# Performance work log

Measured on AMD Instinct MI355X. Metric: run time of the kernel, lower is better.

Reference implementation:

```python
import jax, jax.numpy as jnp
import numpy as np

N, n, m, k = 100000, 32, 16, 32
MU = 100.0  # bubble kernel scale (init arg mu)


def setup_inputs() -> dict:
    key = jax.random.key(0)
    ks = jax.random.split(key, 7)
    x = jax.random.normal(ks[0], (N,), dtype=jnp.float32)
    # torch.nn.Linear(N, n): weight [n, N], bias [n]
    encoder_w = jax.random.normal(ks[1], (n, N), dtype=jnp.float32) / np.float32(np.sqrt(N))
    encoder_b = jnp.zeros((n,), dtype=jnp.float32)
    # decoder parameter [n, N]
    decoder = jax.random.normal(ks[2], (n, N), dtype=jnp.float32) / np.float32(np.sqrt(n))
    # torch.nn.Linear(n, n*m): weight [n*m, n], bias [n*m]
    bw_w = jax.random.normal(ks[3], (n * m, n), dtype=jnp.float32) / np.float32(np.sqrt(n))
    bw_b = jnp.zeros((n * m,), dtype=jnp.float32)
    neighbour_distance = jax.random.uniform(ks[4], (N, k), dtype=jnp.float32)
    neighbour_id = jax.random.randint(ks[5], (N, k), 0, N)
    clustering_labels = jax.random.randint(ks[6], (N,), 0, m)
    return {
        "x": x,
        "encoder_w": encoder_w,
        "encoder_b": encoder_b,
        "decoder": decoder,
        "bw_w": bw_w,
        "bw_b": bw_b,
        "neighbour_distance": neighbour_distance,
        "neighbour_id": neighbour_id,
        "clustering_labels": clustering_labels,
    }


def reference(x, encoder_w, encoder_b, decoder, bw_w, bw_b,
              neighbour_distance, neighbour_id, clustering_labels):
    # encode: [N] -> [n]
    encoded = x @ encoder_w.T + encoder_b
    # per-basis, per-cluster bandwidths: sigmoid(Linear)/60 -> [n, m] -> expand to [n, N]
    bandwidths = jax.nn.sigmoid(encoded @ bw_w.T + bw_b) / 60.0
    w = bandwidths.reshape(n, m)[:, clustering_labels]  # [n, N]
    # bubble window: relu(1 - d^2 / (w*mu)^2) -> [n, N, k]
    window = jax.nn.relu(1.0 - neighbour_distance[None, :, :] ** 2
                         / (w[:, :, None] * MU) ** 2)
    # normalization over axis 1 (the N axis), faithful to the source's dim=1
    window = window / jnp.sum(window, axis=1, keepdims=True)
    # gather decoder rows at neighbours, weight, reduce over k: [n, N]
    convolved_basis = jnp.sum(decoder[:, neighbour_id] * window, axis=-1)
    # [n] @ [n, N] -> [N]
    return encoded @ convolved_basis
```

## Files before the change

kernel.cpp:

```cpp
#include <hip/hip_runtime.h>
#include <hip/hip_fp16.h>

#define N_PTS 100000
#define MU_F  100.0f

typedef unsigned int uint;
typedef _Float16 h2 __attribute__((ext_vector_type(2)));
typedef float f2 __attribute__((ext_vector_type(2)));

#define E_SCALE 16384.0f
#define E_SCALE_INV (1.0f / 16384.0f)

static __device__ inline h2 h2pack(float a, float b) {
    return __builtin_bit_cast(h2, __builtin_amdgcn_cvt_pkrtz(a, b));
}
static __device__ inline float fdot2f(h2 a, h2 b, float c) {
    return __builtin_amdgcn_fdot2(a, b, c, false);
}
static __device__ inline h2 h2fma(h2 a, h2 b, h2 c) {
#if __has_builtin(__builtin_elementwise_fma)
    return __builtin_elementwise_fma(a, b, c);
#else
    return a * b + c;
#endif
}
static __device__ inline h2 h2max(h2 a, h2 b) {
#if __has_builtin(__builtin_elementwise_max)
    return __builtin_elementwise_max(a, b);
#else
    h2 r;
    r.x = a.x > b.x ? a.x : b.x;
    r.y = a.y > b.y ? a.y : b.y;
    return r;
#endif
}

#define ENC_BLKS 256
#define TR_BLKS  1563
#define S_BLKS   1024
#define S_PCH    98
#define NPAIRS   (N_PTS / 2)
#define M_BLKS   2048
#define M_CH     ((NPAIRS + M_BLKS - 1) / M_BLKS)

__global__ __launch_bounds__(256) void k_prep(const float* __restrict__ x,
                                              const float* __restrict__ encW,
                                              const float* __restrict__ encB,
                                              float* __restrict__ enc) {
    int b = blockIdx.x;
    int row = b & 31;
    int chunk = b >> 5;
    const int CH = N_PTS / 8;
    int base = chunk * CH;
    const float4* W4 = reinterpret_cast<const float4*>(encW + (size_t)row * N_PTS + base);
    const float4* x4 = reinterpret_cast<const float4*>(x + base);
    const int nv = CH / 4;
    float acc = 0.f;
    for (int idx = threadIdx.x; idx < nv; idx += 256) {
        float4 w = W4[idx];
        float4 xv = x4[idx];
        acc += w.x * xv.x + w.y * xv.y + w.z * xv.z + w.w * xv.w;
    }
    #pragma unroll
    for (int off = 32; off > 0; off >>= 1) acc += __shfl_down(acc, off);
    __shared__ float sred[4];
    int wid = threadIdx.x >> 6;
    if ((threadIdx.x & 63) == 0) sred[wid] = acc;
    __syncthreads();
    if (threadIdx.x == 0) {
        float s = sred[0] + sred[1] + sred[2] + sred[3];
        if (chunk == 0) s += encB[row];
        atomicAdd(enc + row, s);
    }
}

__global__ __launch_bounds__(256) void k_tab(const float* __restrict__ enc_g,
                                             const float* __restrict__ bw_w,
                                             const float* __restrict__ bw_b,
                                             float* __restrict__ invFG,
                                             h2* __restrict__ invHLG) {
    __shared__ float encL[32];
    __shared__ float invF[512];
    if (threadIdx.x < 32) encL[threadIdx.x] = enc_g[threadIdx.x];
    __syncthreads();
    for (int r = threadIdx.x; r < 512; r += 256) {
        int i = r >> 4, c = r & 15;
        const float4* wr4 = reinterpret_cast<const float4*>(bw_w + (size_t)r * 32);
        float z = bw_b[r];
        #pragma unroll
        for (int p4 = 0; p4 < 8; ++p4) {
            float4 wv = wr4[p4];
            z = fmaf(encL[4 * p4 + 0], wv.x, z);
            z = fmaf(encL[4 * p4 + 1], wv.y, z);
            z = fmaf(encL[4 * p4 + 2], wv.z, z);
            z = fmaf(encL[4 * p4 + 3], wv.w, z);
        }
        float s = 1.f / (1.f + __expf(-z));
        float wmu = s * (MU_F / 60.0f);
        float iv = 1.f / (wmu * wmu);
        invF[c * 32 + i] = iv;
        invFG[c * 32 + i] = iv;
    }
    __syncthreads();
    {
        int t = threadIdx.x;
        int c = t >> 4, q = (t >> 2) & 3, tt = t & 3;
        int i0 = q * 8 + 2 * tt;
        invHLG[t] = h2pack(fminf(invF[c * 32 + i0], 6.0e4f),
                           fminf(invF[c * 32 + i0 + 1], 6.0e4f));
    }
}

__global__ __launch_bounds__(256, 4) void k_S(const float* __restrict__ invFG,
                                              const float* __restrict__ nd,
                                              const int* __restrict__ labels,
                                              float* __restrict__ S,
                                              float* __restrict__ S_part,
                                              const float* __restrict__ dec,
                                              __half* __restrict__ decT) {
    int b = blockIdx.x;
    if (b >= S_BLKS) {
        __shared__ float tile[32][65];
        int j0 = (b - S_BLKS) * 64;
        int col = threadIdx.x & 63;
        int r0 = threadIdx.x >> 6;
        #pragma unroll
        for (int it = 0; it < 8; ++it) {
            int row = it * 4 + r0;
            int j = j0 + col;
            float v = (j < N_PTS) ? dec[(size_t)row * N_PTS + j] : 0.f;
            tile[row][col] = v;
        }
        __syncthreads();
        #pragma unroll
        for (int it = 0; it < 4; ++it) {
            int idx = it * 256 + threadIdx.x;
            int j = idx >> 4;
            int p = idx & 15;
            int jj = j0 + j;
            if (jj < N_PTS) {
                __half2 h = __halves2half2(__float2half(tile[2 * p][j]),
                                           __float2half(tile[2 * p + 1][j]));
                *reinterpret_cast<__half2*>(decT + (size_t)jj * 32 + 2 * p) = h;
            }
        }
        return;
    }

    __shared__ float invF[512];
    if (threadIdx.x < 128)
        reinterpret_cast<float4*>(invF)[threadIdx.x] =
            reinterpret_cast<const float4*>(invFG)[threadIdx.x];
    __syncthreads();

    int kk = threadIdx.x & 31;
    int ig = threadIdx.x >> 5;
    int start = b * S_PCH;
    int jend = min(start + S_PCH, N_PTS);

    float a0 = 0.f, a1 = 0.f, a2 = 0.f, a3 = 0.f;

    auto ld4 = [&](int jbase, float* d, int* cc) {
        #pragma unroll
        for (int u = 0; u < 4; ++u) {
            int j = jbase + u;
            int jc = min(j, N_PTS - 1);
            float dv = nd[(size_t)jc * 32 + kk];
            cc[u] = labels[jc];
            d[u] = (j < jend) ? dv : 1.0e15f;
        }
    };
    float dA[4], dB[4]; int cA[4], cB[4];
    ld4(start, dA, cA);
    for (int jj = start; jj < jend; jj += 4) {
        ld4(jj + 4, dB, cB);
        #pragma unroll
        for (int u = 0; u < 4; ++u) {
            float4 iv = *reinterpret_cast<const float4*>(&invF[cA[u] * 32 + ig * 4]);
            float d2 = dA[u] * dA[u];
            a0 += fmaxf(fmaf(d2, -iv.x, 1.f), 0.f);
            a1 += fmaxf(fmaf(d2, -iv.y, 1.f), 0.f);
            a2 += fmaxf(fmaf(d2, -iv.z, 1.f), 0.f);
            a3 += fmaxf(fmaf(d2, -iv.w, 1.f), 0.f);
        }
        #pragma unroll
        for (int u = 0; u < 4; ++u) { dA[u] = dB[u]; cA[u] = cB[u]; }
    }

    int cell = (ig * 4) * 32 + kk;
    if (S_part) {
        float* dst = S_part + (size_t)b * 1024 + cell;
        dst[0] = a0; dst[32] = a1; dst[64] = a2; dst[96] = a3;
    } else {
        atomicAdd(&S[cell], a0);
        atomicAdd(&S[cell + 32], a1);
        atomicAdd(&S[cell + 64], a2);
        atomicAdd(&S[cell + 96], a3);
    }
}

__global__ __launch_bounds__(1024) void k_S_reduce(const float* __restrict__ S_part,
                                                   float* __restrict__ S) {
    int g = blockIdx.x;
    int t = threadIdx.x;
    float s = 0.f;
    #pragma unroll
    for (int u = 0; u < 16; ++u)
        s += S_part[(size_t)(g * 16 + u) * 1024 + t];
    atomicAdd(&S[t], s);
}

__global__ __launch_bounds__(256) void k_elf(const float* __restrict__ enc_g,
                                             const float* __restrict__ S_g,
                                             h2* __restrict__ EhG_A,
                                             h2* __restrict__ EhG_B) {
    __shared__ float encL[32];
    __shared__ float ELf[1024];
    if (threadIdx.x < 32) encL[threadIdx.x] = enc_g[threadIdx.x];
    __syncthreads();
    for (int t = threadIdx.x; t < 1024; t += 256)
        ELf[t] = encL[t >> 5] / S_g[t] * E_SCALE;
    __syncthreads();
    {
        int t = threadIdx.x;
        int lane = t >> 2, tt = t & 3;
        int R = lane >> 2, q = lane & 3;
        int i0 = q * 8 + 2 * tt;
        EhG_A[t] = h2pack(ELf[i0 * 32 + R],      ELf[(i0 + 1) * 32 + R]);
        EhG_B[t] = h2pack(ELf[i0 * 32 + R + 16], ELf[(i0 + 1) * 32 + R + 16]);
    }
}

__global__ __launch_bounds__(256, 4) void k_main(const h2* __restrict__ invHLG,
                                                 const h2* __restrict__ EhG_A,
                                                 const h2* __restrict__ EhG_B,
                                                 const float* __restrict__ nd,
                                                 const int* __restrict__ nid,
                                                 const int* __restrict__ labels,
                                                 const __half* __restrict__ decT,
                                                 float* __restrict__ out) {
    __shared__ h2 invHL[256];
    if (threadIdx.x < 64)
        reinterpret_cast<uint4*>(invHL)[threadIdx.x] =
            reinterpret_cast<const uint4*>(invHLG)[threadIdx.x];
    __syncthreads();

    int lane = threadIdx.x & 63;
    int R = lane >> 2;
    int q = lane & 3;

    h2 EhA[4], EhB[4];
    {
        uint4 a = reinterpret_cast<const uint4*>(EhG_A)[lane];
        uint4 bq = reinterpret_cast<const uint4*>(EhG_B)[lane];
        EhA[0] = __builtin_bit_cast(h2, a.x);  EhA[1] = __builtin_bit_cast(h2, a.y);
        EhA[2] = __builtin_bit_cast(h2, a.z);  EhA[3] = __builtin_bit_cast(h2, a.w);
        EhB[0] = __builtin_bit_cast(h2, bq.x); EhB[1] = __builtin_bit_cast(h2, bq.y);
        EhB[2] = __builtin_bit_cast(h2, bq.z); EhB[3] = __builtin_bit_cast(h2, bq.w);
    }
    const h2 zero2 = h2pack(0.f, 0.f);
    const h2 one2 = h2pack(1.f, 1.f);

    int w = threadIdx.x >> 6;
    int start = blockIdx.x * M_CH;
    int pend = min(start + M_CH, NPAIRS);
    int pa = start + w;
    const uint4* decQ = reinterpret_cast<const uint4*>(decT);
    if (pa >= pend) return;

    auto load_ldd = [&](int pc, int* id, float* dd, int& c0, int& c1) {
        pc = min(pc, NPAIRS - 1);
        int j0 = 2 * pc, j1 = j0 + 1;
        #pragma unroll
        for (int s = 0; s < 4; ++s) {
            size_t idx = (size_t)((s >> 1) ? j1 : j0) * 32 + (s & 1) * 16 + R;
            id[s] = __builtin_nontemporal_load(&nid[idx]);
            dd[s] = __builtin_nontemporal_load(&nd[idx]);
        }
        c0 = labels[j0];
        c1 = labels[j1];
    };
    auto load_rows = [&](const int* id, uint4* r) {
        #pragma unroll
        for (int s = 0; s < 4; ++s)
            r[s] = decQ[(size_t)id[s] * 4 + q];
    };
    auto load_ih = [&](int c0, int c1, h2* ih0, h2* ih1) {
        uint4 a = *reinterpret_cast<const uint4*>(&invHL[c0 * 16 + q * 4]);
        uint4 bq = *reinterpret_cast<const uint4*>(&invHL[c1 * 16 + q * 4]);
        ih0[0] = __builtin_bit_cast(h2, a.x);  ih0[1] = __builtin_bit_cast(h2, a.y);
        ih0[2] = __builtin_bit_cast(h2, a.z);  ih0[3] = __builtin_bit_cast(h2, a.w);
        ih1[0] = __builtin_bit_cast(h2, bq.x); ih1[1] = __builtin_bit_cast(h2, bq.y);
        ih1[2] = __builtin_bit_cast(h2, bq.z); ih1[3] = __builtin_bit_cast(h2, bq.w);
    };

    int ida[4], idb[4]; float dda[4], ddb[4];
    int ca0, ca1, cb0, cb1;
    uint4 ra[4], rb[4];
    h2 ihA0[4], ihA1[4];

    load_ldd(pa, ida, dda, ca0, ca1);
    load_ldd(pa + 4, idb, ddb, cb0, cb1);
    load_rows(ida, ra);
    load_ih(ca0, ca1, ihA0, ihA1);

    while (pa < pend) {
        load_rows(idb, rb);
        h2 ihB0[4], ihB1[4];
        load_ih(cb0, cb1, ihB0, ihB1);
        int idc[4]; float ddc[4]; int cc0, cc1;
        load_ldd(pa + 8, idc, ddc, cc0, cc1);
        __builtin_amdgcn_sched_barrier(0);

        float d20 = dda[0] * dda[0];
        float d21 = dda[1] * dda[1];
        float d22 = dda[2] * dda[2];
        float d23 = dda[3] * dda[3];
        h2 md0 = h2pack(-d20, -d20);
        h2 md1 = h2pack(-d21, -d21);
        h2 md2 = h2pack(-d22, -d22);
        h2 md3 = h2pack(-d23, -d23);

        float a0 = 0.f, a1 = 0.f, a2 = 0.f, a3 = 0.f;
        #pragma unroll
        for (int t = 0; t < 4; ++t) {
            uint dw0 = (t == 0) ? ra[0].x : (t == 1) ? ra[0].y : (t == 2) ? ra[0].z : ra[0].w;
            uint dw1 = (t == 0) ? ra[1].x : (t == 1) ? ra[1].y : (t == 2) ? ra[1].z : ra[1].w;
            uint dw2 = (t == 0) ? ra[2].x : (t == 1) ? ra[2].y : (t == 2) ? ra[2].z : ra[2].w;
            uint dw3 = (t == 0) ? ra[3].x : (t == 1) ? ra[3].y : (t == 2) ? ra[3].z : ra[3].w;
            {
                h2 wv = h2max(h2fma(md0, ihA0[t], one2), zero2);
                a0 = fdot2f(wv * EhA[t], __builtin_bit_cast(h2, dw0), a0);
            }
            {
                h2 wv = h2max(h2fma(md1, ihA0[t], one2), zero2);
                a1 = fdot2f(wv * EhB[t], __builtin_bit_cast(h2, dw1), a1);
            }
            {
                h2 wv = h2max(h2fma(md2, ihA1[t], one2), zero2);
                a2 = fdot2f(wv * EhA[t], __builtin_bit_cast(h2, dw2), a2);
            }
            {
                h2 wv = h2max(h2fma(md3, ihA1[t], one2), zero2);
                a3 = fdot2f(wv * EhB[t], __builtin_bit_cast(h2, dw3), a3);
            }
        }
        float u = a0 + a1;
        float v = a2 + a3;
        #pragma unroll
        for (int off = 32; off > 0; off >>= 1) {
            u += __shfl_xor(u, off);
            v += __shfl_xor(v, off);
        }
        if (lane == 0)  out[2 * pa]     = u * E_SCALE_INV;
        if (lane == 32) out[2 * pa + 1] = v * E_SCALE_INV;

        ca0 = cb0; ca1 = cb1; cb0 = cc0; cb1 = cc1;
        #pragma unroll
        for (int s = 0; s < 4; ++s) {
            dda[s] = ddb[s]; ddb[s] = ddc[s];
            ida[s] = idb[s]; idb[s] = idc[s];
            ra[s] = rb[s];
            ihA0[s] = ihB0[s]; ihA1[s] = ihB1[s];
        }
        pa += 4;
    }
}

extern "C" void kernel_launch(void* const* d_in, const int* in_sizes, int n_in,
                              void* d_out, int out_size, void* d_ws, size_t ws_size,
                              hipStream_t stream) {
    const float* x     = (const float*)d_in[0];
    const float* enc_w = (const float*)d_in[1];
    const float* enc_b = (const float*)d_in[2];
    const float* dec   = (const float*)d_in[3];
    const float* bw_w  = (const float*)d_in[4];
    const float* bw_b  = (const float*)d_in[5];
    const float* nd    = (const float*)d_in[6];
    const int*   nid   = (const int*)d_in[7];
    const int*   labels= (const int*)d_in[8];
    float* out = (float*)d_out;

    char* ws = (char*)d_ws;
    float* enc    = (float*)(ws + 0);
    float* S      = (float*)(ws + 128);
    float* invFG  = (float*)(ws + 4224);
    h2*    invHLG = (h2*)(ws + 6272);
    h2*    EhG_A  = (h2*)(ws + 7296);
    h2*    EhG_B  = (h2*)(ws + 8320);
    __half* decT  = (__half*)(ws + 532480);
    bool use_part = ws_size >= 11126784ull;
    float* S_part = use_part ? (float*)(ws + 6932480) : nullptr;

    (void)hipMemsetAsync(d_ws, 0, 4224, stream);
    k_prep<<<dim3(ENC_BLKS), dim3(256), 0, stream>>>(x, enc_w, enc_b, enc);
    k_tab<<<dim3(1), dim3(256), 0, stream>>>(enc, bw_w, bw_b, invFG, invHLG);
    k_S<<<dim3(S_BLKS + TR_BLKS), dim3(256), 0, stream>>>(
        invFG, nd, labels, S, S_part, dec, decT);
    if (use_part)
        k_S_reduce<<<dim3(64), dim3(1024), 0, stream>>>(S_part, S);
    k_elf<<<dim3(1), dim3(256), 0, stream>>>(enc, S, EhG_A, EhG_B);
    k_main<<<dim3(M_BLKS), dim3(256), 0, stream>>>(invHLG, EhG_A, EhG_B,
                                                   nd, nid, labels, decT, out);
}
```

Before: 174.7 us.

## Fuse tiny prep kernels via last-block-done counters to cut launches

```diff
diff --git a/kernel.cpp b/kernel.cpp
--- a/kernel.cpp
+++ b/kernel.cpp
@@ -43,10 +43,17 @@
 #define M_BLKS   2048
 #define M_CH     ((NPAIRS + M_BLKS - 1) / M_BLKS)
 
-__global__ __launch_bounds__(256) void k_prep(const float* __restrict__ x,
-                                              const float* __restrict__ encW,
-                                              const float* __restrict__ encB,
-                                              float* __restrict__ enc) {
+
+__global__ __launch_bounds__(256) void k_prep_tab(const float* __restrict__ x,
+                                                  const float* __restrict__ encW,
+                                                  const float* __restrict__ encB,
+                                                  const float* __restrict__ bw_w,
+                                                  const float* __restrict__ bw_b,
+                                                  float* __restrict__ enc,
+                                                  float* __restrict__ enc_part,
+                                                  int* __restrict__ doneA,
+                                                  float* __restrict__ invFG,
+                                                  h2* __restrict__ invHLG) {
     int b = blockIdx.x;
     int row = b & 31;
     int chunk = b >> 5;
@@ -64,24 +71,31 @@
     #pragma unroll
     for (int off = 32; off > 0; off >>= 1) acc += __shfl_down(acc, off);
     __shared__ float sred[4];
+    __shared__ int sLast;
     int wid = threadIdx.x >> 6;
     if ((threadIdx.x & 63) == 0) sred[wid] = acc;
     __syncthreads();
     if (threadIdx.x == 0) {
         float s = sred[0] + sred[1] + sred[2] + sred[3];
         if (chunk == 0) s += encB[row];
-        atomicAdd(enc + row, s);
-    }
-}
-
-__global__ __launch_bounds__(256) void k_tab(const float* __restrict__ enc_g,
-                                             const float* __restrict__ bw_w,
-                                             const float* __restrict__ bw_b,
-                                             float* __restrict__ invFG,
-                                             h2* __restrict__ invHLG) {
+        atomicExch(&enc_part[b], s);
+        __threadfence();
+        int old = atomicAdd(doneA, 1);
+        sLast = (old == ENC_BLKS - 1);
+    }
+    __syncthreads();
+    if (!sLast) return;
+
     __shared__ float encL[32];
     __shared__ float invF[512];
-    if (threadIdx.x < 32) encL[threadIdx.x] = enc_g[threadIdx.x];
+    if (threadIdx.x < 32) {
+        float s = 0.f;
+        #pragma unroll
+        for (int c = 0; c < 8; ++c)
+            s += atomicAdd(&enc_part[(c << 5) | threadIdx.x], 0.f);
+        encL[threadIdx.x] = s;
+        enc[threadIdx.x] = s;
+    }
     __syncthreads();
     for (int r = threadIdx.x; r < 512; r += 256) {
         int i = r >> 4, c = r & 15;
@@ -111,13 +125,16 @@
     }
 }
 
-__global__ __launch_bounds__(256, 4) void k_S(const float* __restrict__ invFG,
-                                              const float* __restrict__ nd,
-                                              const int* __restrict__ labels,
-                                              float* __restrict__ S,
-                                              float* __restrict__ S_part,
-                                              const float* __restrict__ dec,
-                                              __half* __restrict__ decT) {
+__global__ __launch_bounds__(256, 4) void k_S_all(const float* __restrict__ invFG,
+                                                  const float* __restrict__ nd,
+                                                  const int* __restrict__ labels,
+                                                  float* __restrict__ S,
+                                                  int* __restrict__ doneB,
+                                                  const float* __restrict__ enc_g,
+                                                  h2* __restrict__ EhG_A,
+                                                  h2* __restrict__ EhG_B,
+                                                  const float* __restrict__ dec,
+                                                  __half* __restrict__ decT) {
     int b = blockIdx.x;
     if (b >= S_BLKS) {
         __shared__ float tile[32][65];
@@ -148,6 +165,7 @@
     }
 
     __shared__ float invF[512];
+    __shared__ int sLast;
     if (threadIdx.x < 128)
         reinterpret_cast<float4*>(invF)[threadIdx.x] =
             reinterpret_cast<const float4*>(invFG)[threadIdx.x];
@@ -188,38 +206,26 @@
     }
 
     int cell = (ig * 4) * 32 + kk;
-    if (S_part) {
-        float* dst = S_part + (size_t)b * 1024 + cell;
-        dst[0] = a0; dst[32] = a1; dst[64] = a2; dst[96] = a3;
-    } else {
-        atomicAdd(&S[cell], a0);
-        atomicAdd(&S[cell + 32], a1);
-        atomicAdd(&S[cell + 64], a2);
-        atomicAdd(&S[cell + 96], a3);
-    }
-}
-
-__global__ __launch_bounds__(1024) void k_S_reduce(const float* __restrict__ S_part,
-                                                   float* __restrict__ S) {
-    int g = blockIdx.x;
-    int t = threadIdx.x;
-    float s = 0.f;
-    #pragma unroll
-    for (int u = 0; u < 16; ++u)
-        s += S_part[(size_t)(g * 16 + u) * 1024 + t];
-    atomicAdd(&S[t], s);
-}
-
-__global__ __launch_bounds__(256) void k_elf(const float* __restrict__ enc_g,
-                                             const float* __restrict__ S_g,
-                                             h2* __restrict__ EhG_A,
-                                             h2* __restrict__ EhG_B) {
+    atomicAdd(&S[cell], a0);
+    atomicAdd(&S[cell + 32], a1);
+    atomicAdd(&S[cell + 64], a2);
+    atomicAdd(&S[cell + 96], a3);
+    __threadfence();
+    if (threadIdx.x == 0) {
+        int old = atomicAdd(doneB, 1);
+        sLast = (old == S_BLKS - 1);
+    }
+    __syncthreads();
+    if (!sLast) return;
+
     __shared__ float encL[32];
     __shared__ float ELf[1024];
     if (threadIdx.x < 32) encL[threadIdx.x] = enc_g[threadIdx.x];
     __syncthreads();
-    for (int t = threadIdx.x; t < 1024; t += 256)
-        ELf[t] = encL[t >> 5] / S_g[t] * E_SCALE;
+    for (int t = threadIdx.x; t < 1024; t += 256) {
+        float Sv = atomicAdd(&S[t], 0.f);
+        ELf[t] = encL[t >> 5] / Sv * E_SCALE;
+    }
     __syncthreads();
     {
         int t = threadIdx.x;
@@ -382,24 +388,22 @@
     float* out = (float*)d_out;
 
     char* ws = (char*)d_ws;
-    float* enc    = (float*)(ws + 0);
-    float* S      = (float*)(ws + 128);
-    float* invFG  = (float*)(ws + 4224);
-    h2*    invHLG = (h2*)(ws + 6272);
-    h2*    EhG_A  = (h2*)(ws + 7296);
-    h2*    EhG_B  = (h2*)(ws + 8320);
-    __half* decT  = (__half*)(ws + 532480);
-    bool use_part = ws_size >= 11126784ull;
-    float* S_part = use_part ? (float*)(ws + 6932480) : nullptr;
+    float* S        = (float*)(ws + 0);
+    int*   doneA    = (int*)(ws + 4096);
+    int*   doneB    = (int*)(ws + 4100);
+    float* enc      = (float*)(ws + 4224);
+    float* enc_part = (float*)(ws + 4352);
+    float* invFG    = (float*)(ws + 5376);
+    h2*    invHLG   = (h2*)(ws + 7424);
+    h2*    EhG_A    = (h2*)(ws + 8448);
+    h2*    EhG_B    = (h2*)(ws + 9472);
+    __half* decT    = (__half*)(ws + 532480);
 
     (void)hipMemsetAsync(d_ws, 0, 4224, stream);
-    k_prep<<<dim3(ENC_BLKS), dim3(256), 0, stream>>>(x, enc_w, enc_b, enc);
-    k_tab<<<dim3(1), dim3(256), 0, stream>>>(enc, bw_w, bw_b, invFG, invHLG);
-    k_S<<<dim3(S_BLKS + TR_BLKS), dim3(256), 0, stream>>>(
-        invFG, nd, labels, S, S_part, dec, decT);
-    if (use_part)
-        k_S_reduce<<<dim3(64), dim3(1024), 0, stream>>>(S_part, S);
-    k_elf<<<dim3(1), dim3(256), 0, stream>>>(enc, S, EhG_A, EhG_B);
+    k_prep_tab<<<dim3(ENC_BLKS), dim3(256), 0, stream>>>(
+        x, enc_w, enc_b, bw_w, bw_b, enc, enc_part, doneA, invFG, invHLG);
+    k_S_all<<<dim3(S_BLKS + TR_BLKS), dim3(256), 0, stream>>>(
+        invFG, nd, labels, S, doneB, enc, EhG_A, EhG_B, dec, decT);
     k_main<<<dim3(M_BLKS), dim3(256), 0, stream>>>(invHLG, EhG_A, EhG_B,
                                                    nd, nid, labels, decT, out);
 }
```

After: 233.7 us. 33.7% more time.
